# Optimization experiments

Hardware: AMD Instinct MI355X
Metric: run time of the kernel (lower is better)

## Reference

```python
import jax, jax.numpy as jnp
import numpy as np

N_HEAD = 16
N_KV_HEAD = 4
N_EMBD = 2048

def rotate_half(x):
    x1, x2 = jnp.split(x, 2, axis=-1)
    return jnp.concatenate([-x2, x1], axis=-1)

def rope_tables(T, k):
    # angles = 10000^(-2*i/k) for i in [0, k/2); cos/sin repeated twice along last dim
    inv = jnp.power(10000.0, -2.0 * jnp.arange(k // 2, dtype=jnp.float32) / k)
    ang = jnp.arange(T, dtype=jnp.float32)[:, None] * inv[None, :]  # [T, k/2]
    cos = jnp.tile(jnp.cos(ang), (1, 2))  # [T, k]
    sin = jnp.tile(jnp.sin(ang), (1, 2))
    return cos, sin

def setup_inputs() -> dict:
    key = jax.random.key(0)
    ks = jax.random.split(key, 5)
    B, T, D = 4, 1024, N_EMBD
    g, h = N_KV_HEAD, N_HEAD
    k = D // h
    s = 0.02
    return {
        'x': jax.random.normal(ks[0], (B, T, D), dtype=jnp.float32),
        'Wq': jax.random.normal(ks[1], (D, D), dtype=jnp.float32) * s,
        'Wk': jax.random.normal(ks[2], (D, g * k), dtype=jnp.float32) * s,
        'Wv': jax.random.normal(ks[3], (D, g * k), dtype=jnp.float32) * s,
        'Wo': jax.random.normal(ks[4], (D, D), dtype=jnp.float32) * s,
    }

def reference(x, Wq, Wk, Wv, Wo):
    B, T, D = x.shape
    h, g = N_HEAD, N_KV_HEAD
    k = D // h
    Q = (x @ Wq).reshape(B, T, h, k).transpose(0, 2, 1, 3)  # [B,h,T,k]
    K = (x @ Wk).reshape(B, T, g, k).transpose(0, 2, 1, 3)  # [B,g,T,k]
    V = (x @ Wv).reshape(B, T, g, k).transpose(0, 2, 1, 3)
    # GQA: repeat_interleave kv heads to match query heads
    K = jnp.repeat(K, h // g, axis=1)  # [B,h,T,k]
    V = jnp.repeat(V, h // g, axis=1)
    cos, sin = rope_tables(T, k)
    cos = cos[None, None]  # [1,1,T,k]
    sin = sin[None, None]
    Q = Q * cos + rotate_half(Q) * sin
    K = K * cos + rotate_half(K) * sin
    scores = jnp.einsum('bhqk,bhsk->bhqs', Q, K) / jnp.sqrt(jnp.float32(k))
    causal = jnp.tril(jnp.ones((T, T), dtype=bool))
    scores = jnp.where(causal[None, None], scores, -jnp.inf)
    A = jax.nn.softmax(scores, axis=-1)
    Y = jnp.einsum('bhqs,bhsk->bhqk', A, V)
    Y = Y.transpose(0, 2, 1, 3).reshape(B, T, D)
    return Y @ Wo
```

## Files before the change

### kernel.cpp

```cpp
#include <hip/hip_runtime.h>
#include <math.h>

#define B_ 4
#define T_ 1024
#define D_ 2048
#define NH 16
#define NKV 4
#define HD 128
#define KV_D 512
#define QKV_S 2560

typedef __attribute__((ext_vector_type(8))) short short8;
typedef __attribute__((ext_vector_type(4))) float f32x4;

__device__ __forceinline__ ushort f2b(float f) {
    unsigned u = __float_as_uint(f);
    return (ushort)((u + 0x7fffu + ((u >> 16) & 1u)) >> 16);
}
__device__ __forceinline__ float b2f(ushort u) {
    return __uint_as_float((unsigned)u << 16);
}

#if __has_builtin(__builtin_amdgcn_exp2f)
#define EXP2F(x) __builtin_amdgcn_exp2f(x)
#else
#define EXP2F(x) __expf((x) * 0.6931471805599453f)
#endif

#define ASYNC_COPY16(g, l)                                                  \
    __builtin_amdgcn_global_load_lds(                                       \
        (const __attribute__((address_space(1))) void*)(g),                 \
        (__attribute__((address_space(3))) void*)(l), 16, 0, 0)

#define SCHED0() __builtin_amdgcn_sched_barrier(0)
#define SBAR() __builtin_amdgcn_s_barrier()
#define WAITVN(n) asm volatile("s_waitcnt vmcnt(" #n ")" ::: "memory")
#define LGKM0()                                                             \
    do {                                                                    \
        asm volatile("s_waitcnt lgkmcnt(0)" ::: "memory");                  \
        __builtin_amdgcn_sched_barrier(0);                                  \
    } while (0)
#define MFMA16(ap, bp, cc) cc = __builtin_amdgcn_mfma_f32_16x16x32_bf16(ap, bp, cc, 0, 0, 0)

__global__ __launch_bounds__(256) void prep_all(const float* __restrict__ x,
                                                const float* __restrict__ Wq,
                                                const float* __restrict__ Wk,
                                                const float* __restrict__ Wv,
                                                const float* __restrict__ Wo,
                                                ushort* __restrict__ xb,
                                                ushort* __restrict__ WqkvT,
                                                ushort* __restrict__ WoT,
                                                float2* __restrict__ tab) {
    __shared__ float tile[32][33];
    const int bid = blockIdx.x;
    if (bid < 8192) {
        const int i = bid * 256 + threadIdx.x;
        const float4 v = ((const float4*)x)[i];
        ushort4 u;
        u.x = f2b(v.x); u.y = f2b(v.y); u.z = f2b(v.z); u.w = f2b(v.w);
        ((ushort4*)xb)[i] = u;
        return;
    }
    if (bid >= 18432) {
        const int idx = (bid - 18432) * 256 + threadIdx.x;
        const int t = idx >> 6, i = idx & 63;
        const float inv = exp2f((float)i * (-13.287712379549449f / 64.0f));
        const float ang = (float)t * inv;
        tab[idx] = make_float2(cosf(ang), sinf(ang));
        return;
    }
    const float* W;
    ushort* WT;
    int N, rb;
    if (bid < 12288)      { W = Wq; WT = WqkvT;                           N = D_;   rb = bid - 8192; }
    else if (bid < 13312) { W = Wk; WT = WqkvT + (size_t)D_ * D_;         N = KV_D; rb = bid - 12288; }
    else if (bid < 14336) { W = Wv; WT = WqkvT + (size_t)(D_+KV_D) * D_;  N = KV_D; rb = bid - 13312; }
    else                  { W = Wo; WT = WoT;                             N = D_;   rb = bid - 14336; }
    const int bxn = N / 32;
    const int n0 = (rb % bxn) * 32, k0 = (rb / bxn) * 32;
    const int tx = threadIdx.x & 31, ty = threadIdx.x >> 5;
    for (int i = ty; i < 32; i += 8)
        tile[i][tx] = W[(size_t)(k0 + i) * N + n0 + tx];
    __syncthreads();
    for (int i = ty; i < 32; i += 8)
        WT[(size_t)(n0 + i) * D_ + k0 + tx] = f2b(tile[tx][i]);
}

__global__ __launch_bounds__(512, 2) void gemm_qkv256(const ushort* __restrict__ A,
                                                      const ushort* __restrict__ BT,
                                                      ushort* __restrict__ QKV,
                                                      ushort* __restrict__ Vt,
                                                      const float2* __restrict__ tab) {
    extern __shared__ ushort smem[];
    const int K = D_;
    const int NT = K / 64;
    const int tid = threadIdx.x;
    const int m0 = blockIdx.y * 256, n0 = blockIdx.x * 256;
    const int wave = tid >> 6, lane = tid & 63;
    const int wr = wave >> 2, wc = wave & 3;
    const int ln = lane & 15, quad = lane >> 4;

    const int rl = tid >> 3;
    const int cus = ((tid & 7) * 8) ^ ((rl & 7) << 3);
    const ushort* Ag = A + (size_t)(m0 + rl) * K + cus;
    const ushort* Bg = BT + (size_t)(n0 + rl) * K + cus;
    ushort* const stA = smem + tid * 8;
    ushort* const stB = smem + 32768 + tid * 8;

    const int cq0 = (quad * 8) ^ ((ln & 7) << 3);
    const int abase0 = wr * 8192 + ln * 64;
    const int bbase0 = 32768 + (wc >> 1) * 8192 + ((wc & 1) * 64 + ln) * 64;

    f32x4 acc[8][4];
    const f32x4 zero = {0.f, 0.f, 0.f, 0.f};
#pragma unroll
    for (int i = 0; i < 8; ++i)
#pragma unroll
        for (int j = 0; j < 4; ++j) acc[i][j] = zero;

    short8 a[4][2], b0[2][2], b1[2][2];

#define GLOADS(dnoff, koff)                                                 \
    do {                                                                    \
        const ushort* Agk = Ag + (koff);                                    \
        const ushort* Bgk = Bg + (koff);                                    \
        ASYNC_COPY16(Agk,                    stA + (dnoff));                \
        ASYNC_COPY16(Agk + (size_t)64 * K,   stA + (dnoff) + 4096);         \
        ASYNC_COPY16(Agk + (size_t)128 * K,  stA + (dnoff) + 8192);         \
        ASYNC_COPY16(Agk + (size_t)192 * K,  stA + (dnoff) + 12288);        \
        ASYNC_COPY16(Bgk,                    stB + (dnoff));                \
        ASYNC_COPY16(Bgk + (size_t)64 * K,   stB + (dnoff) + 4096);         \
        ASYNC_COPY16(Bgk + (size_t)128 * K,  stB + (dnoff) + 8192);         \
        ASYNC_COPY16(Bgk + (size_t)192 * K,  stB + (dnoff) + 12288);        \
    } while (0)

#define READ_A(dst, base, roff)                                             \
    _Pragma("unroll")                                                       \
    for (int mt = 0; mt < 4; ++mt) {                                        \
        dst[mt][0] = *(const short8*)&smem[(base) + (roff) + mt * 1024 + cq0];        \
        dst[mt][1] = *(const short8*)&smem[(base) + (roff) + mt * 1024 + (cq0 ^ 32)]; \
    }
#define READ_B(dst, base, noff)                                             \
    _Pragma("unroll")                                                       \
    for (int nt = 0; nt < 2; ++nt) {                                        \
        dst[nt][0] = *(const short8*)&smem[(base) + (noff) + nt * 1024 + cq0];        \
        dst[nt][1] = *(const short8*)&smem[(base) + (noff) + nt * 1024 + (cq0 ^ 32)]; \
    }
#define QUAD_MMA(ar, br, mo, no)                                            \
    _Pragma("unroll")                                                       \
    for (int mt = 0; mt < 4; ++mt)                                          \
        _Pragma("unroll")                                                   \
        for (int nt = 0; nt < 2; ++nt) {                                    \
            MFMA16(ar[mt][0], br[nt][0], acc[(mo) + mt][(no) + nt]);        \
            MFMA16(ar[mt][1], br[nt][1], acc[(mo) + mt][(no) + nt]);        \
        }

    GLOADS(0, 0);
    GLOADS(16384, 64);

#pragma unroll 1
    for (int t = 0; t < NT; ++t) {
        const int cb = (t & 1) * 16384;

        if (t + 1 < NT) { WAITVN(8); } else { WAITVN(0); }
        SBAR();
        SCHED0();

        READ_A(a, abase0 + cb, 0);
        READ_B(b0, bbase0 + cb, 0);
        READ_B(b1, bbase0 + cb, 2048);

        __builtin_amdgcn_s_setprio(1);
        QUAD_MMA(a, b0, 0, 0);
        QUAD_MMA(a, b1, 0, 2);
        __builtin_amdgcn_s_setprio(0);

        READ_A(a, abase0 + cb, 4096);
        LGKM0();
        SBAR();
        if (t + 2 < NT) GLOADS(cb, (t + 2) * 64);
        SCHED0();
        __builtin_amdgcn_s_setprio(1);
        QUAD_MMA(a, b1, 4, 2);
        QUAD_MMA(a, b0, 4, 0);
        __builtin_amdgcn_s_setprio(0);
    }
#undef GLOADS
#undef READ_A
#undef READ_B
#undef QUAD_MMA

    __syncthreads();
    ushort* Epi = smem;
    const int b = m0 >> 10;
    const int t0 = m0 & 1023;
    const int hid0 = n0 >> 7;

    for (int hh = 0; hh < 2; ++hh) {
        if ((wc >> 1) == hh) {
            const int cb2 = (wc & 1) * 64;
#pragma unroll
            for (int am = 0; am < 8; ++am)
#pragma unroll
                for (int an = 0; an < 4; ++an)
#pragma unroll
                    for (int r = 0; r < 4; ++r)
                        Epi[(wr * 128 + am * 16 + quad * 4 + r) * 136 + cb2 + an * 16 + ln] =
                            f2b(acc[am][an][r]);
        }
        __syncthreads();

        const int hid = hid0 + hh;
        if (hid < NH + NKV) {
            const bool isQ = hid < NH;
            const size_t colbase = isQ ? (size_t)hid * HD : (size_t)D_ + (size_t)(hid - NH) * HD;
            const float sc = isQ ? (0.08838834764831845f * 1.4426950408889634f) : 1.0f;
            const int r = tid >> 1;
            const int hf = tid & 1;
            const int tt = t0 + r;
            ushort* orow = QKV + (size_t)(m0 + r) * QKV_S + colbase;
            const float4* tab4 = (const float4*)tab;
#pragma unroll
            for (int jj = 0; jj < 4; ++jj) {
                const int dbase = hf * 32 + jj * 8;
                const short8 lo = *(const short8*)&Epi[r * 136 + dbase];
                const short8 hi = *(const short8*)&Epi[r * 136 + 64 + dbase];
                ushort olo[8], ohi[8];
#pragma unroll
                for (int kq = 0; kq < 4; ++kq) {
                    const float4 cs = tab4[((tt * 64 + dbase) >> 1) + kq];
                    const float x1a = b2f(lo[2 * kq]),     x2a = b2f(hi[2 * kq]);
                    const float x1b = b2f(lo[2 * kq + 1]), x2b = b2f(hi[2 * kq + 1]);
                    olo[2 * kq]     = f2b((x1a * cs.x - x2a * cs.y) * sc);
                    ohi[2 * kq]     = f2b((x2a * cs.x + x1a * cs.y) * sc);
                    olo[2 * kq + 1] = f2b((x1b * cs.z - x2b * cs.w) * sc);
                    ohi[2 * kq + 1] = f2b((x2b * cs.z + x1b * cs.w) * sc);
                }
                *(short8*)&orow[dbase]      = *(short8*)olo;
                *(short8*)&orow[dbase + 64] = *(short8*)ohi;
            }
        } else {
            const int kv = hid - (NH + NKV);
            const int dd = tid & 127;
            const int th = tid >> 7;
            ushort* vrow = Vt + ((size_t)((b * NKV + kv) * HD + dd)) * T_ + t0 + th * 64;
#pragma unroll
            for (int jj = 0; jj < 8; ++jj) {
                ushort pk[8];
#pragma unroll
                for (int k2 = 0; k2 < 8; ++k2)
                    pk[k2] = Epi[(th * 64 + jj * 8 + k2) * 136 + dd];
                *(short8*)&vrow[jj * 8] = *(short8*)pk;
            }
        }
        __syncthreads();
    }
}

__global__ __launch_bounds__(256) void gemm_bf16(const ushort* __restrict__ A,
                                                 const ushort* __restrict__ BT,
                                                 float* __restrict__ C,
                                                 int M, int N, int K) {
    __shared__ ushort As[128 * 32];
    __shared__ ushort Bs[128 * 32];
    const int tid = threadIdx.x;
    const int m0 = blockIdx.y * 128, n0 = blockIdx.x * 128;
    const int wave = tid >> 6, lane = tid & 63;
    const int wm = (wave >> 1) * 64, wn = (wave & 1) * 64;
    const int lrow = lane & 15;
    const int quad = lane >> 4;

    f32x4 acc[4][4];
    const f32x4 zero = {0.f, 0.f, 0.f, 0.f};
#pragma unroll
    for (int i = 0; i < 4; ++i)
#pragma unroll
        for (int j = 0; j < 4; ++j) acc[i][j] = zero;

    const int srow = tid >> 2;
    const int scol = (tid & 3) * 8;
    const ushort* Ag = A + (size_t)(m0 + srow) * K + scol;
    const ushort* Bg = BT + (size_t)(n0 + srow) * K + scol;
    ushort* AsT = As + tid * 8;
    ushort* BsT = Bs + tid * 8;

    for (int k0 = 0; k0 < K; k0 += 32) {
        ASYNC_COPY16(Ag + k0, AsT);
        ASYNC_COPY16(Ag + k0 + (size_t)64 * K, AsT + 64 * 32);
        ASYNC_COPY16(Bg + k0, BsT);
        ASYNC_COPY16(Bg + k0 + (size_t)64 * K, BsT + 64 * 32);
        __syncthreads();

        short8 a[4], b[4];
#pragma unroll
        for (int mt = 0; mt < 4; ++mt)
            a[mt] = *(const short8*)&As[(wm + mt * 16 + lrow) * 32 + quad * 8];
#pragma unroll
        for (int nt = 0; nt < 4; ++nt)
            b[nt] = *(const short8*)&Bs[(wn + nt * 16 + lrow) * 32 + quad * 8];
#pragma unroll
        for (int mt = 0; mt < 4; ++mt)
#pragma unroll
            for (int nt = 0; nt < 4; ++nt)
                acc[mt][nt] = __builtin_amdgcn_mfma_f32_16x16x32_bf16(
                    a[mt], b[nt], acc[mt][nt], 0, 0, 0);
        __syncthreads();
    }

    const int crow = quad * 4;
    const int ccol = lrow;
#pragma unroll
    for (int mt = 0; mt < 4; ++mt)
#pragma unroll
        for (int nt = 0; nt < 4; ++nt)
#pragma unroll
            for (int r = 0; r < 4; ++r)
                C[(size_t)(m0 + wm + mt * 16 + crow + r) * N +
                  n0 + wn + nt * 16 + ccol] = acc[mt][nt][r];
}

__global__ __launch_bounds__(256) void attn_mfma(const ushort* __restrict__ QKV,
                                                 const ushort* __restrict__ Vt,
                                                 ushort* __restrict__ Yb) {
    __shared__ ushort Ks[64][136];
    __shared__ ushort Vs[128][72];
    __shared__ ushort Ps[4][16][72];

    const int bh = blockIdx.x;
    const int qt = (int)gridDim.y - 1 - (int)blockIdx.y;
    const int b = bh >> 4, h = bh & 15;
    const int kvh = h >> 2;
    const int q0 = qt * 64;
    const int tid = threadIdx.x;
    const int wave = tid >> 6, lane = tid & 63;
    const int ln = lane & 15, quad = lane >> 4;

    short8 qf[4];
    {
        const ushort* qp = QKV + ((size_t)(b * T_ + q0 + wave * 16 + ln)) * QKV_S + h * HD + quad * 8;
#pragma unroll
        for (int f = 0; f < 4; ++f) qf[f] = *(const short8*)(qp + f * 32);
    }

    f32x4 acc[8];
    const f32x4 zero = {0.f, 0.f, 0.f, 0.f};
#pragma unroll
    for (int j = 0; j < 8; ++j) acc[j] = zero;
    float m_r[4], l_r[4];
#pragma unroll
    for (int r = 0; r < 4; ++r) { m_r[r] = -INFINITY; l_r[r] = 0.f; }

    const int qrow = q0 + wave * 16 + quad * 4;

    for (int kt = 0; kt <= qt; ++kt) {
        const int s0 = kt * 64;
        __syncthreads();
#pragma unroll
        for (int c = 0; c < 4; ++c) {
            const int cid = tid + 256 * c;
            const int s = cid >> 4, ch = cid & 15;
            *(short8*)&Ks[s][ch * 8] =
                *(const short8*)&QKV[((size_t)(b * T_ + s0 + s)) * QKV_S + D_ + kvh * HD + ch * 8];
        }
#pragma unroll
        for (int c = 0; c < 4; ++c) {
            const int cid = tid + 256 * c;
            const int d = cid >> 3, ch = cid & 7;
            *(short8*)&Vs[d][ch * 8] =
                *(const short8*)&Vt[((size_t)((b * NKV + kvh) * HD + d)) * T_ + s0 + ch * 8];
        }
        __syncthreads();

        float sc[4][4];
#pragma unroll
        for (int ct = 0; ct < 4; ++ct) {
            f32x4 s4 = zero;
#pragma unroll
            for (int f = 0; f < 4; ++f)
                s4 = __builtin_amdgcn_mfma_f32_16x16x32_bf16(
                    qf[f], *(const short8*)&Ks[ct * 16 + ln][f * 32 + quad * 8], s4, 0, 0, 0);
#pragma unroll
            for (int r = 0; r < 4; ++r) sc[ct][r] = s4[r];
        }
        if (kt == qt) {
#pragma unroll
            for (int ct = 0; ct < 4; ++ct)
#pragma unroll
                for (int r = 0; r < 4; ++r)
                    if (s0 + ct * 16 + ln > qrow + r) sc[ct][r] = -INFINITY;
        }
        float alpha[4];
#pragma unroll
        for (int r = 0; r < 4; ++r) {
            float mx = fmaxf(fmaxf(sc[0][r], sc[1][r]), fmaxf(sc[2][r], sc[3][r]));
            mx = fmaxf(mx, __shfl_xor(mx, 1));
            mx = fmaxf(mx, __shfl_xor(mx, 2));
            mx = fmaxf(mx, __shfl_xor(mx, 4));
            mx = fmaxf(mx, __shfl_xor(mx, 8));
            const float mnew = fmaxf(m_r[r], mx);
            alpha[r] = EXP2F(m_r[r] - mnew);
            m_r[r] = mnew;
#pragma unroll
            for (int ct = 0; ct < 4; ++ct) sc[ct][r] = EXP2F(sc[ct][r] - mnew);
            float sum = (sc[0][r] + sc[1][r]) + (sc[2][r] + sc[3][r]);
            sum += __shfl_xor(sum, 1);
            sum += __shfl_xor(sum, 2);
            sum += __shfl_xor(sum, 4);
            sum += __shfl_xor(sum, 8);
            l_r[r] = l_r[r] * alpha[r] + sum;
        }
#pragma unroll
        for (int ct = 0; ct < 4; ++ct)
#pragma unroll
            for (int r = 0; r < 4; ++r)
                Ps[wave][quad * 4 + r][ct * 16 + ln] = f2b(sc[ct][r]);
#pragma unroll
        for (int j = 0; j < 8; ++j)
#pragma unroll
            for (int r = 0; r < 4; ++r) acc[j][r] *= alpha[r];
        const short8 pa0 = *(const short8*)&Ps[wave][ln][quad * 8];
        const short8 pa1 = *(const short8*)&Ps[wave][ln][32 + quad * 8];
#pragma unroll
        for (int j = 0; j < 8; ++j) {
            acc[j] = __builtin_amdgcn_mfma_f32_16x16x32_bf16(
                pa0, *(const short8*)&Vs[j * 16 + ln][quad * 8], acc[j], 0, 0, 0);
            acc[j] = __builtin_amdgcn_mfma_f32_16x16x32_bf16(
                pa1, *(const short8*)&Vs[j * 16 + ln][32 + quad * 8], acc[j], 0, 0, 0);
        }
    }

    float invl[4];
#pragma unroll
    for (int r = 0; r < 4; ++r) invl[r] = 1.f / l_r[r];
    ushort* yb = Yb + ((size_t)(b * T_ + qrow)) * D_ + h * HD + ln;
#pragma unroll
    for (int r = 0; r < 4; ++r)
#pragma unroll
        for (int j = 0; j < 8; ++j)
            yb[(size_t)r * D_ + j * 16] = f2b(acc[j][r] * invl[r]);
}

extern "C" void kernel_launch(void* const* d_in, const int* in_sizes, int n_in,
                              void* d_out, int out_size, void* d_ws, size_t ws_size,
                              hipStream_t stream) {
    const float* x  = (const float*)d_in[0];
    const float* Wq = (const float*)d_in[1];
    const float* Wk = (const float*)d_in[2];
    const float* Wv = (const float*)d_in[3];
    const float* Wo = (const float*)d_in[4];
    float* out = (float*)d_out;

    char* w = (char*)d_ws;
    ushort* xb    = (ushort*)w;  w += (size_t)4096 * D_ * 2;
    ushort* WqkvT = (ushort*)w;  w += (size_t)3072 * D_ * 2;
    ushort* QKV   = (ushort*)w;  w += (size_t)4096 * QKV_S * 2;
    ushort* Vt    = (ushort*)w;  w += (size_t)B_ * KV_D * T_ * 2;
    ushort* Yb    = (ushort*)w;  w += (size_t)4096 * D_ * 2;
    ushort* WoT   = (ushort*)w;  w += (size_t)D_ * D_ * 2;
    float2* tab   = (float2*)w;  w += (size_t)T_ * 64 * 8;

    const int M = B_ * T_;
    dim3 blk(256);

    hipFuncSetAttribute(reinterpret_cast<const void*>(gemm_qkv256),
                        hipFuncAttributeMaxDynamicSharedMemorySize, 131072);

    prep_all<<<18688, blk, 0, stream>>>(x, Wq, Wk, Wv, Wo, xb, WqkvT, WoT, tab);

    gemm_qkv256<<<dim3(3072 / 256, M / 256), dim3(512), 131072, stream>>>(xb, WqkvT, QKV, Vt, tab);

    attn_mfma<<<dim3(B_ * NH, T_ / 64), blk, 0, stream>>>(QKV, Vt, Yb);

    gemm_bf16<<<dim3(D_ / 128, M / 128), blk, 0, stream>>>(Yb, WoT, out, M, D_, D_);
}
```

Baseline: 301.4 us.

## Retune all four kernels: wider transpose tiles, split QKV MMA phases, K64 GEMM, KV prefetch

The weight transpose in prep uses 64x64 tiles with float4 loads and 16-byte bf16 stores, cutting the block count and widening memory accesses. The QKV GEMM main loop is split into more phases with extra LDS waits and barriers between MFMA groups. The output GEMM moves to a K-step of 64 with an XOR-swizzled LDS layout, halving the number of loop iterations and barriers. The attention kernel prefetches the next K/V tile into registers while the current tile is computed and raises wave priority around the MFMA blocks. The extra barriers in the QKV GEMM could serialise waves, and the register prefetch in attention raises register pressure.

```diff
diff --git a/kernel.cpp b/kernel.cpp
--- a/kernel.cpp
+++ b/kernel.cpp
@@ -32,6 +32,7 @@
         (const __attribute__((address_space(1))) void*)(g),                 \
         (__attribute__((address_space(3))) void*)(l), 16, 0, 0)
 
+#define MFMA16(ap, bp, cc) cc = __builtin_amdgcn_mfma_f32_16x16x32_bf16(ap, bp, cc, 0, 0, 0)
 #define SCHED0() __builtin_amdgcn_sched_barrier(0)
 #define SBAR() __builtin_amdgcn_s_barrier()
 #define WAITVN(n) asm volatile("s_waitcnt vmcnt(" #n ")" ::: "memory")
@@ -40,7 +41,6 @@
         asm volatile("s_waitcnt lgkmcnt(0)" ::: "memory");                  \
         __builtin_amdgcn_sched_barrier(0);                                  \
     } while (0)
-#define MFMA16(ap, bp, cc) cc = __builtin_amdgcn_mfma_f32_16x16x32_bf16(ap, bp, cc, 0, 0, 0)
 
 __global__ __launch_bounds__(256) void prep_all(const float* __restrict__ x,
                                                 const float* __restrict__ Wq,
@@ -51,18 +51,19 @@
                                                 ushort* __restrict__ WqkvT,
                                                 ushort* __restrict__ WoT,
                                                 float2* __restrict__ tab) {
-    __shared__ float tile[32][33];
+    __shared__ float tile[64][65];
     const int bid = blockIdx.x;
+    const int tid = threadIdx.x;
     if (bid < 8192) {
-        const int i = bid * 256 + threadIdx.x;
+        const int i = bid * 256 + tid;
         const float4 v = ((const float4*)x)[i];
         ushort4 u;
         u.x = f2b(v.x); u.y = f2b(v.y); u.z = f2b(v.z); u.w = f2b(v.w);
         ((ushort4*)xb)[i] = u;
         return;
     }
-    if (bid >= 18432) {
-        const int idx = (bid - 18432) * 256 + threadIdx.x;
+    if (bid >= 10752) {
+        const int idx = (bid - 10752) * 256 + tid;
         const int t = idx >> 6, i = idx & 63;
         const float inv = exp2f((float)i * (-13.287712379549449f / 64.0f));
         const float ang = (float)t * inv;
@@ -72,18 +73,30 @@
     const float* W;
     ushort* WT;
     int N, rb;
-    if (bid < 12288)      { W = Wq; WT = WqkvT;                           N = D_;   rb = bid - 8192; }
-    else if (bid < 13312) { W = Wk; WT = WqkvT + (size_t)D_ * D_;         N = KV_D; rb = bid - 12288; }
-    else if (bid < 14336) { W = Wv; WT = WqkvT + (size_t)(D_+KV_D) * D_;  N = KV_D; rb = bid - 13312; }
-    else                  { W = Wo; WT = WoT;                             N = D_;   rb = bid - 14336; }
-    const int bxn = N / 32;
-    const int n0 = (rb % bxn) * 32, k0 = (rb / bxn) * 32;
-    const int tx = threadIdx.x & 31, ty = threadIdx.x >> 5;
-    for (int i = ty; i < 32; i += 8)
-        tile[i][tx] = W[(size_t)(k0 + i) * N + n0 + tx];
+    if (bid < 9216)      { W = Wq; WT = WqkvT;                           N = D_;   rb = bid - 8192; }
+    else if (bid < 9472) { W = Wk; WT = WqkvT + (size_t)D_ * D_;         N = KV_D; rb = bid - 9216; }
+    else if (bid < 9728) { W = Wv; WT = WqkvT + (size_t)(D_+KV_D) * D_;  N = KV_D; rb = bid - 9472; }
+    else                 { W = Wo; WT = WoT;                             N = D_;   rb = bid - 9728; }
+    const int bxn = N / 64;
+    const int n0 = (rb % bxn) * 64, k0 = (rb / bxn) * 64;
+    const int tx = tid & 15, ty = tid >> 4;
+#pragma unroll
+    for (int i = 0; i < 4; ++i) {
+        const int r = ty + i * 16;
+        const float4 v = *(const float4*)&W[(size_t)(k0 + r) * N + n0 + tx * 4];
+        tile[r][tx * 4 + 0] = v.x;
+        tile[r][tx * 4 + 1] = v.y;
+        tile[r][tx * 4 + 2] = v.z;
+        tile[r][tx * 4 + 3] = v.w;
+    }
     __syncthreads();
-    for (int i = ty; i < 32; i += 8)
-        WT[(size_t)(n0 + i) * D_ + k0 + tx] = f2b(tile[tx][i]);
+    const int n = tid >> 2, ch = (tid & 3) * 16;
+    ushort tmp[16];
+#pragma unroll
+    for (int j = 0; j < 16; ++j) tmp[j] = f2b(tile[ch + j][n]);
+    ushort* orow = WT + (size_t)(n0 + n) * D_ + k0 + ch;
+    *(short8*)&orow[0] = *(short8*)&tmp[0];
+    *(short8*)&orow[8] = *(short8*)&tmp[8];
 }
 
 __global__ __launch_bounds__(512, 2) void gemm_qkv256(const ushort* __restrict__ A,
@@ -168,12 +181,18 @@
 
         READ_A(a, abase0 + cb, 0);
         READ_B(b0, bbase0 + cb, 0);
-        READ_B(b1, bbase0 + cb, 2048);
-
+        LGKM0();
         __builtin_amdgcn_s_setprio(1);
         QUAD_MMA(a, b0, 0, 0);
+        __builtin_amdgcn_s_setprio(0);
+        SBAR();
+
+        READ_B(b1, bbase0 + cb, 2048);
+        LGKM0();
+        __builtin_amdgcn_s_setprio(1);
         QUAD_MMA(a, b1, 0, 2);
         __builtin_amdgcn_s_setprio(0);
+        SBAR();
 
         READ_A(a, abase0 + cb, 4096);
         LGKM0();
@@ -182,6 +201,10 @@
         SCHED0();
         __builtin_amdgcn_s_setprio(1);
         QUAD_MMA(a, b1, 4, 2);
+        __builtin_amdgcn_s_setprio(0);
+        SBAR();
+
+        __builtin_amdgcn_s_setprio(1);
         QUAD_MMA(a, b0, 4, 0);
         __builtin_amdgcn_s_setprio(0);
     }
@@ -261,8 +284,8 @@
                                                  const ushort* __restrict__ BT,
                                                  float* __restrict__ C,
                                                  int M, int N, int K) {
-    __shared__ ushort As[128 * 32];
-    __shared__ ushort Bs[128 * 32];
+    __shared__ ushort As[128 * 64];
+    __shared__ ushort Bs[128 * 64];
     const int tid = threadIdx.x;
     const int m0 = blockIdx.y * 128, n0 = blockIdx.x * 128;
     const int wave = tid >> 6, lane = tid & 63;
@@ -277,33 +300,38 @@
 #pragma unroll
         for (int j = 0; j < 4; ++j) acc[i][j] = zero;
 
-    const int srow = tid >> 2;
-    const int scol = (tid & 3) * 8;
+    const int srow = tid >> 3;
+    const int scol = ((tid & 7) * 8) ^ ((srow & 7) << 3);
     const ushort* Ag = A + (size_t)(m0 + srow) * K + scol;
     const ushort* Bg = BT + (size_t)(n0 + srow) * K + scol;
     ushort* AsT = As + tid * 8;
     ushort* BsT = Bs + tid * 8;
-
-    for (int k0 = 0; k0 < K; k0 += 32) {
-        ASYNC_COPY16(Ag + k0, AsT);
-        ASYNC_COPY16(Ag + k0 + (size_t)64 * K, AsT + 64 * 32);
-        ASYNC_COPY16(Bg + k0, BsT);
-        ASYNC_COPY16(Bg + k0 + (size_t)64 * K, BsT + 64 * 32);
+    const int swr = (lrow & 7) << 3;
+
+    for (int k0 = 0; k0 < K; k0 += 64) {
+#pragma unroll
+        for (int c = 0; c < 4; ++c) {
+            ASYNC_COPY16(Ag + k0 + (size_t)(c * 32) * K, AsT + c * 2048);
+            ASYNC_COPY16(Bg + k0 + (size_t)(c * 32) * K, BsT + c * 2048);
+        }
         __syncthreads();
 
-        short8 a[4], b[4];
-#pragma unroll
-        for (int mt = 0; mt < 4; ++mt)
-            a[mt] = *(const short8*)&As[(wm + mt * 16 + lrow) * 32 + quad * 8];
-#pragma unroll
-        for (int nt = 0; nt < 4; ++nt)
-            b[nt] = *(const short8*)&Bs[(wn + nt * 16 + lrow) * 32 + quad * 8];
-#pragma unroll
-        for (int mt = 0; mt < 4; ++mt)
+#pragma unroll
+        for (int ks = 0; ks < 2; ++ks) {
+            const int col = (quad * 8) ^ (ks * 32) ^ swr;
+            short8 a[4], b[4];
+#pragma unroll
+            for (int mt = 0; mt < 4; ++mt)
+                a[mt] = *(const short8*)&As[(wm + mt * 16 + lrow) * 64 + col];
 #pragma unroll
             for (int nt = 0; nt < 4; ++nt)
-                acc[mt][nt] = __builtin_amdgcn_mfma_f32_16x16x32_bf16(
-                    a[mt], b[nt], acc[mt][nt], 0, 0, 0);
+                b[nt] = *(const short8*)&Bs[(wn + nt * 16 + lrow) * 64 + col];
+#pragma unroll
+            for (int mt = 0; mt < 4; ++mt)
+#pragma unroll
+                for (int nt = 0; nt < 4; ++nt)
+                    MFMA16(a[mt], b[nt], acc[mt][nt]);
+        }
         __syncthreads();
     }
 
@@ -342,6 +370,27 @@
         for (int f = 0; f < 4; ++f) qf[f] = *(const short8*)(qp + f * 32);
     }
 
+    const size_t kv_row = (size_t)((b * NKV + kvh) * HD);
+    const ushort* const Vbase = Vt + kv_row * T_;
+    const ushort* const Kbase = QKV + ((size_t)(b * T_)) * QKV_S + D_ + kvh * HD;
+
+    short8 kreg[4], vreg[4];
+#define LOAD_KV(s0_)                                                        \
+    do {                                                                    \
+        _Pragma("unroll")                                                   \
+        for (int c = 0; c < 4; ++c) {                                       \
+            const int cid = tid + 256 * c;                                  \
+            const int s = cid >> 4, ch = cid & 15;                          \
+            kreg[c] = *(const short8*)&Kbase[((size_t)((s0_) + s)) * QKV_S + ch * 8]; \
+        }                                                                   \
+        _Pragma("unroll")                                                   \
+        for (int c = 0; c < 4; ++c) {                                       \
+            const int cid = tid + 256 * c;                                  \
+            const int d = cid >> 3, ch = cid & 7;                           \
+            vreg[c] = *(const short8*)&Vbase[(size_t)d * T_ + (s0_) + ch * 8]; \
+        }                                                                   \
+    } while (0)
+
     f32x4 acc[8];
     const f32x4 zero = {0.f, 0.f, 0.f, 0.f};
 #pragma unroll
@@ -351,6 +400,8 @@
     for (int r = 0; r < 4; ++r) { m_r[r] = -INFINITY; l_r[r] = 0.f; }
 
     const int qrow = q0 + wave * 16 + quad * 4;
+
+    LOAD_KV(0);
 
     for (int kt = 0; kt <= qt; ++kt) {
         const int s0 = kt * 64;
@@ -359,19 +410,20 @@
         for (int c = 0; c < 4; ++c) {
             const int cid = tid + 256 * c;
             const int s = cid >> 4, ch = cid & 15;
-            *(short8*)&Ks[s][ch * 8] =
-                *(const short8*)&QKV[((size_t)(b * T_ + s0 + s)) * QKV_S + D_ + kvh * HD + ch * 8];
+            *(short8*)&Ks[s][ch * 8] = kreg[c];
         }
 #pragma unroll
         for (int c = 0; c < 4; ++c) {
             const int cid = tid + 256 * c;
             const int d = cid >> 3, ch = cid & 7;
-            *(short8*)&Vs[d][ch * 8] =
-                *(const short8*)&Vt[((size_t)((b * NKV + kvh) * HD + d)) * T_ + s0 + ch * 8];
+            *(short8*)&Vs[d][ch * 8] = vreg[c];
         }
         __syncthreads();
 
+        if (kt < qt) LOAD_KV(s0 + 64);
+
         float sc[4][4];
+        __builtin_amdgcn_s_setprio(1);
 #pragma unroll
         for (int ct = 0; ct < 4; ++ct) {
             f32x4 s4 = zero;
@@ -382,6 +434,7 @@
 #pragma unroll
             for (int r = 0; r < 4; ++r) sc[ct][r] = s4[r];
         }
+        __builtin_amdgcn_s_setprio(0);
         if (kt == qt) {
 #pragma unroll
             for (int ct = 0; ct < 4; ++ct)
@@ -420,6 +473,7 @@
             for (int r = 0; r < 4; ++r) acc[j][r] *= alpha[r];
         const short8 pa0 = *(const short8*)&Ps[wave][ln][quad * 8];
         const short8 pa1 = *(const short8*)&Ps[wave][ln][32 + quad * 8];
+        __builtin_amdgcn_s_setprio(1);
 #pragma unroll
         for (int j = 0; j < 8; ++j) {
             acc[j] = __builtin_amdgcn_mfma_f32_16x16x32_bf16(
@@ -427,7 +481,9 @@
             acc[j] = __builtin_amdgcn_mfma_f32_16x16x32_bf16(
                 pa1, *(const short8*)&Vs[j * 16 + ln][32 + quad * 8], acc[j], 0, 0, 0);
         }
-    }
+        __builtin_amdgcn_s_setprio(0);
+    }
+#undef LOAD_KV
 
     float invl[4];
 #pragma unroll
@@ -465,7 +521,7 @@
     hipFuncSetAttribute(reinterpret_cast<const void*>(gemm_qkv256),
                         hipFuncAttributeMaxDynamicSharedMemorySize, 131072);
 
-    prep_all<<<18688, blk, 0, stream>>>(x, Wq, Wk, Wv, Wo, xb, WqkvT, WoT, tab);
+    prep_all<<<11008, blk, 0, stream>>>(x, Wq, Wk, Wv, Wo, xb, WqkvT, WoT, tab);
 
     gemm_qkv256<<<dim3(3072 / 256, M / 256), dim3(512), 131072, stream>>>(xb, WqkvT, QKV, Vt, tab);
 
```

After: 284.7 us. 1.06x faster.
